# Optimization experiments

Measured on AMD Instinct MI355X. Metric: run time of the kernel, lower is better.

The kernel has to match this reference:

```python
import jax, jax.numpy as jnp
import numpy as np

KERNELS = (9, 7, 5, 3)


def setup_inputs() -> dict:
    key = jax.random.key(0)
    ks = jax.random.split(key, 10)
    Nx = Ny = 512
    D = 256
    C = 8192
    H = 1024
    T = 5
    S = len(KERNELS)
    sc = 0.05
    node_emb = jax.random.normal(ks[0], (Nx * Ny, D), jnp.float32)
    tile_ids = jax.random.randint(ks[1], (C,), 0, Nx * Ny)
    cm = jax.random.randint(ks[2], (C, T), 0, 2, dtype=jnp.int32)
    create_mask = cm.at[:, 0].set(1)  # guarantee every city is eligible
    return dict(
        node_emb=node_emb,
        conv_W0=jax.random.normal(ks[3], (S, D, D), jnp.float32) * sc,
        conv_b0=jnp.zeros((S, D), jnp.float32),
        conv_W1=jax.random.normal(ks[4], (S, D, D), jnp.float32) * sc,
        conv_b1=jnp.zeros((S, D), jnp.float32),
        mlp_W0=jax.random.normal(ks[5], (D * (1 + S), H), jnp.float32) * sc,
        mlp_b0=jnp.zeros((H,), jnp.float32),
        mlp_W1=jax.random.normal(ks[6], (H, H), jnp.float32) * sc,
        mlp_b1=jnp.zeros((H,), jnp.float32),
        mlp_W2=jax.random.normal(ks[7], (H, T), jnp.float32) * sc,
        mlp_b2=jnp.zeros((T,), jnp.float32),
        tile_ids=tile_ids,
        create_mask=create_mask,
        Nx=Nx,
        Ny=Ny,
    )


def _forward(node_emb, conv_W0, conv_b0, conv_W1, conv_b1,
             mlp_W0, mlp_b0, mlp_W1, mlp_b1, mlp_W2, mlp_b2,
             tile_ids, create_mask, Nx, Ny):
    D = node_emb.shape[1]
    rmax = max(KERNELS) // 2
    # zero-padded spatial grid, matching F.unfold with padding=k//2
    grid = node_emb.reshape(Nx, Ny, D)
    padded = jnp.pad(grid, ((rmax, rmax), (rmax, rmax), (0, 0)))
    Wp = Ny + 2 * rmax
    pf = padded.reshape(-1, D)  # (padded_tiles, D)
    x = tile_ids // Ny
    y = tile_ids % Ny
    feats = [node_emb[tile_ids]]  # (C, D) raw city embedding
    for s, k in enumerate(KERNELS):
        r = k // 2
        off = jnp.arange(-r, r + 1)
        ix = x[:, None, None] + off[None, :, None] + rmax  # (C,k,1)
        iy = y[:, None, None] + off[None, None, :] + rmax  # (C,1,k)
        flat = ix * Wp + iy  # (C,k,k)
        pooled = pf[flat].mean(axis=(1, 2))  # (C,D) mean-pooled patch
        h = jax.nn.relu(pooled @ conv_W0[s] + conv_b0[s])
        h = h @ conv_W1[s] + conv_b1[s]  # n_conv_layers=2 projection
        feats.append(h)
    combined = jnp.concatenate(feats, axis=-1)  # (C, D*(1+S))
    h = jax.nn.relu(combined @ mlp_W0 + mlp_b0)
    h = jax.nn.relu(h @ mlp_W1 + mlp_b1)
    logits = h @ mlp_W2 + mlp_b2  # (C, T)
    mask = create_mask > 0
    # stable masked softmax
    neg_inf = jnp.array(-jnp.inf, logits.dtype)
    m = jnp.max(jnp.where(mask, logits, neg_inf), axis=-1, keepdims=True)
    e = jnp.where(mask, jnp.exp(logits - m), 0.0)
    probs = e / jnp.sum(e, axis=-1, keepdims=True)
    safe = jnp.clip(probs, 1e-8, None)
    entropies = -jnp.sum(probs * jnp.log(safe), axis=-1)
    logits_masked = jnp.where(mask, logits, neg_inf)
    return probs, entropies, logits_masked, mask


def reference(node_emb, conv_W0, conv_b0, conv_W1, conv_b1,
              mlp_W0, mlp_b0, mlp_W1, mlp_b1, mlp_W2, mlp_b2,
              tile_ids, create_mask, Nx, Ny):
    return _forward(node_emb, conv_W0, conv_b0, conv_W1, conv_b1,
                    mlp_W0, mlp_b0, mlp_W1, mlp_b1, mlp_W2, mlp_b2,
                    tile_ids, create_mask, Nx, Ny)
```

## Files before the change

kernel.cpp:

```cpp
#include <hip/hip_runtime.h>
#include <hip/hip_bf16.h>
#include <math.h>
#include <float.h>

#define NX 512
#define NY 512
#define DIM 256
#define CITIES 8192
#define HID 1024
#define TT 5
#define NS 4
#define COMB (DIM * (1 + NS))

typedef unsigned short u16;
typedef __attribute__((ext_vector_type(8))) short short8;
typedef __attribute__((ext_vector_type(8))) unsigned short ushort8;
typedef __attribute__((ext_vector_type(4))) float f32x4;

__device__ __forceinline__ u16 f2bf(float f) {
    __hip_bfloat16 h = __float2bfloat16(f);
    return __builtin_bit_cast(u16, h);
}
__device__ __forceinline__ float bf2f(u16 u) {
    __hip_bfloat16 h = __builtin_bit_cast(__hip_bfloat16, u);
    return __bfloat162float(h);
}

__global__ __launch_bounds__(256)
void transpose_bf16(const float* __restrict__ in, u16* __restrict__ out,
                    int K, int N) {
    __shared__ float tile[32][33];
    const int s = blockIdx.z;
    in  += (size_t)s * K * N;
    out += (size_t)s * K * N;
    const int bn = blockIdx.x * 32, bk = blockIdx.y * 32;
    const int tx = threadIdx.x & 31, ty = threadIdx.x >> 5;
#pragma unroll
    for (int i = 0; i < 32; i += 8)
        tile[ty + i][tx] = in[(size_t)(bk + ty + i) * N + bn + tx];
    __syncthreads();
#pragma unroll
    for (int i = 0; i < 32; i += 8)
        out[(size_t)(bn + ty + i) * K + bk + tx] = f2bf(tile[tx][ty + i]);
}

__global__ void pool_kernel(const float* __restrict__ node_emb,
                            const int* __restrict__ tile_ids,
                            u16* __restrict__ P,
                            u16* __restrict__ combined) {
    int c = blockIdx.x;
    int d = threadIdx.x;
    int tile = tile_ids[c];
    int x = tile >> 9;
    int y = tile & 511;
    float s3 = 0.f, s5 = 0.f, s7 = 0.f, s9 = 0.f, center = 0.f;
#pragma unroll
    for (int dx = -4; dx <= 4; ++dx) {
        int gx = x + dx;
        bool okx = ((unsigned)gx < (unsigned)NX);
#pragma unroll
        for (int dy = -4; dy <= 4; ++dy) {
            int gy = y + dy;
            float v = 0.f;
            if (okx && ((unsigned)gy < (unsigned)NY)) {
                v = node_emb[(size_t)((gx << 9) + gy) * DIM + d];
            }
            s9 += v;
            const int ax = dx < 0 ? -dx : dx;
            const int ay = dy < 0 ? -dy : dy;
            if (ax <= 3 && ay <= 3) s7 += v;
            if (ax <= 2 && ay <= 2) s5 += v;
            if (ax <= 1 && ay <= 1) s3 += v;
            if (dx == 0 && dy == 0) center = v;
        }
    }
    combined[(size_t)c * COMB + d] = f2bf(center);
    P[((size_t)c * NS + 0) * DIM + d] = f2bf(s9 * (1.f / 81.f));
    P[((size_t)c * NS + 1) * DIM + d] = f2bf(s7 * (1.f / 49.f));
    P[((size_t)c * NS + 2) * DIM + d] = f2bf(s5 * (1.f / 25.f));
    P[((size_t)c * NS + 3) * DIM + d] = f2bf(s3 * (1.f / 9.f));
}

__global__ __launch_bounds__(256)
void gemm_bf16(const u16* __restrict__ A, int lda, long aZ,
               const u16* __restrict__ BT, int ldb, long bZ,
               const float* __restrict__ bias, long biasZ,
               u16* __restrict__ C, int ldc, long cZ,
               int K, int relu) {
    __shared__ u16 ldsA[128 * 64];
    __shared__ u16 ldsB[128 * 64];
    A    += (size_t)blockIdx.z * aZ;
    BT   += (size_t)blockIdx.z * bZ;
    bias += (size_t)blockIdx.z * biasZ;
    C    += (size_t)blockIdx.z * cZ;

    const int t    = threadIdx.x;
    const int lane = t & 63;
    const int wid  = t >> 6;
    const int wm   = wid >> 1;
    const int wn   = wid & 1;
    const int m0   = blockIdx.y * 128;
    const int n0   = blockIdx.x * 128;

    const int srow0 = wid * 32 + (lane >> 3);
    const int c7    = lane & 7;
    const int fr    = lane & 15;
    const int kq    = lane >> 4;

    f32x4 acc[4][4];
#pragma unroll
    for (int m = 0; m < 4; ++m)
#pragma unroll
        for (int n = 0; n < 4; ++n) acc[m][n] = (f32x4){0.f, 0.f, 0.f, 0.f};

    for (int k0 = 0; k0 < K; k0 += 64) {
        __syncthreads();
#pragma unroll
        for (int i = 0; i < 4; ++i) {
            const int row = srow0 + i * 8;
            const int sc  = c7 ^ (row & 7);
            const u16* ga = A + (size_t)(m0 + row) * lda + k0 + sc * 8;
            __builtin_amdgcn_global_load_lds(
                (const __attribute__((address_space(1))) void*)ga,
                (__attribute__((address_space(3))) void*)(ldsA + (wid * 32 + i * 8) * 64),
                16, 0, 0);
        }
#pragma unroll
        for (int i = 0; i < 4; ++i) {
            const int row = srow0 + i * 8;
            const int sc  = c7 ^ (row & 7);
            const u16* gb = BT + (size_t)(n0 + row) * ldb + k0 + sc * 8;
            __builtin_amdgcn_global_load_lds(
                (const __attribute__((address_space(1))) void*)gb,
                (__attribute__((address_space(3))) void*)(ldsB + (wid * 32 + i * 8) * 64),
                16, 0, 0);
        }
        __syncthreads();

#pragma unroll
        for (int kk = 0; kk < 2; ++kk) {
            short8 af[4], bfr[4];
#pragma unroll
            for (int m = 0; m < 4; ++m) {
                const int r  = wm * 64 + m * 16 + fr;
                const int ck = (kk * 4 + kq) ^ (r & 7);
                af[m] = *(const short8*)(ldsA + r * 64 + ck * 8);
            }
#pragma unroll
            for (int n = 0; n < 4; ++n) {
                const int r  = wn * 64 + n * 16 + fr;
                const int ck = (kk * 4 + kq) ^ (r & 7);
                bfr[n] = *(const short8*)(ldsB + r * 64 + ck * 8);
            }
#pragma unroll
            for (int m = 0; m < 4; ++m)
#pragma unroll
                for (int n = 0; n < 4; ++n)
                    acc[m][n] = __builtin_amdgcn_mfma_f32_16x16x32_bf16(
                        af[m], bfr[n], acc[m][n], 0, 0, 0);
        }
    }

#pragma unroll
    for (int n = 0; n < 4; ++n) {
        const int col = n0 + wn * 64 + n * 16 + fr;
        const float bv = bias[col];
#pragma unroll
        for (int m = 0; m < 4; ++m) {
            const int row = m0 + wm * 64 + m * 16 + kq * 4;
#pragma unroll
            for (int r = 0; r < 4; ++r) {
                float v = acc[m][n][r] + bv;
                if (relu) v = fmaxf(v, 0.f);
                C[(size_t)(row + r) * ldc + col] = f2bf(v);
            }
        }
    }
}

__global__ __launch_bounds__(256)
void logits_kernel(const u16* __restrict__ g2,
                   const float* __restrict__ W2,
                   const float* __restrict__ b2,
                   float* __restrict__ logits) {
    int row  = blockIdx.x * 4 + (threadIdx.x >> 6);
    int lane = threadIdx.x & 63;
    const u16* gr = g2 + (size_t)row * HID + lane * 16;
    ushort8 v0 = *(const ushort8*)(gr);
    ushort8 v1 = *(const ushort8*)(gr + 8);
    float acc[TT] = {0.f, 0.f, 0.f, 0.f, 0.f};
    const int kbase = lane * 16;
#pragma unroll
    for (int e = 0; e < 8; ++e) {
        float g = bf2f(v0[e]);
#pragma unroll
        for (int tt = 0; tt < TT; ++tt) acc[tt] += g * W2[(kbase + e) * TT + tt];
    }
#pragma unroll
    for (int e = 0; e < 8; ++e) {
        float g = bf2f(v1[e]);
#pragma unroll
        for (int tt = 0; tt < TT; ++tt) acc[tt] += g * W2[(kbase + 8 + e) * TT + tt];
    }
#pragma unroll
    for (int off = 32; off > 0; off >>= 1) {
#pragma unroll
        for (int tt = 0; tt < TT; ++tt)
            acc[tt] += __shfl_down(acc[tt], off, 64);
    }
    if (lane == 0) {
#pragma unroll
        for (int tt = 0; tt < TT; ++tt)
            logits[(size_t)row * TT + tt] = acc[tt] + b2[tt];
    }
}

__global__ void softmax_kernel(const float* __restrict__ logits,
                               const int* __restrict__ create_mask,
                               float* __restrict__ out) {
    int c = blockIdx.x * blockDim.x + threadIdx.x;
    if (c >= CITIES) return;
    float l[TT];
    int mk[TT];
#pragma unroll
    for (int tt = 0; tt < TT; ++tt) {
        l[tt] = logits[(size_t)c * TT + tt];
        mk[tt] = create_mask[(size_t)c * TT + tt];
    }
    float m = -INFINITY;
#pragma unroll
    for (int tt = 0; tt < TT; ++tt)
        if (mk[tt]) m = fmaxf(m, l[tt]);
    float e[TT];
    float s = 0.f;
#pragma unroll
    for (int tt = 0; tt < TT; ++tt) {
        e[tt] = mk[tt] ? expf(l[tt] - m) : 0.f;
        s += e[tt];
    }
    float inv = 1.f / s;
    float ent = 0.f;
    float* probs   = out;
    float* entrop  = out + (size_t)5 * CITIES;
    float* lmasked = out + (size_t)6 * CITIES;
    float* maskout = out + (size_t)11 * CITIES;
#pragma unroll
    for (int tt = 0; tt < TT; ++tt) {
        float p = e[tt] * inv;
        probs[(size_t)c * TT + tt] = p;
        ent -= p * logf(fmaxf(p, 1e-8f));
        lmasked[(size_t)c * TT + tt] = mk[tt] ? l[tt] : -1e30f;
        maskout[(size_t)c * TT + tt] = mk[tt] ? 1.f : 0.f;
    }
    entrop[c] = ent;
}

extern "C" void kernel_launch(void* const* d_in, const int* in_sizes, int n_in,
                              void* d_out, int out_size, void* d_ws, size_t ws_size,
                              hipStream_t stream) {
    const float* node_emb = (const float*)d_in[0];
    const float* conv_W0  = (const float*)d_in[1];
    const float* conv_b0  = (const float*)d_in[2];
    const float* conv_W1  = (const float*)d_in[3];
    const float* conv_b1  = (const float*)d_in[4];
    const float* mlp_W0   = (const float*)d_in[5];
    const float* mlp_b0   = (const float*)d_in[6];
    const float* mlp_W1   = (const float*)d_in[7];
    const float* mlp_b1   = (const float*)d_in[8];
    const float* mlp_W2   = (const float*)d_in[9];
    const float* mlp_b2   = (const float*)d_in[10];
    const int*   tile_ids = (const int*)d_in[11];
    const int*   cmask    = (const int*)d_in[12];
    float* out = (float*)d_out;

    char* w = (char*)d_ws;
    u16* P_bf   = (u16*)w;                    w += (size_t)CITIES * NS * DIM * 2;
    u16* comb   = (u16*)w;                    w += (size_t)CITIES * COMB * 2;
    u16* h0     = (u16*)w;                    w += (size_t)CITIES * NS * DIM * 2;
    u16* g1     = (u16*)w;                    w += (size_t)CITIES * HID * 2;
    u16* g2     = (u16*)w;                    w += (size_t)CITIES * HID * 2;
    u16* W0T    = (u16*)w;                    w += (size_t)NS * DIM * DIM * 2;
    u16* W1T    = (u16*)w;                    w += (size_t)NS * DIM * DIM * 2;
    u16* Wm0T   = (u16*)w;                    w += (size_t)HID * COMB * 2;
    u16* Wm1T   = (u16*)w;                    w += (size_t)HID * HID * 2;
    float* logits = (float*)w;                w += (size_t)CITIES * TT * 4;

    transpose_bf16<<<dim3(DIM/32, DIM/32, NS), 256, 0, stream>>>(conv_W0, W0T, DIM, DIM);
    transpose_bf16<<<dim3(DIM/32, DIM/32, NS), 256, 0, stream>>>(conv_W1, W1T, DIM, DIM);
    transpose_bf16<<<dim3(HID/32, COMB/32, 1), 256, 0, stream>>>(mlp_W0, Wm0T, COMB, HID);
    transpose_bf16<<<dim3(HID/32, HID/32, 1), 256, 0, stream>>>(mlp_W1, Wm1T, HID, HID);

    pool_kernel<<<CITIES, DIM, 0, stream>>>(node_emb, tile_ids, P_bf, comb);

    gemm_bf16<<<dim3(DIM/128, CITIES/128, NS), 256, 0, stream>>>(
        P_bf, NS * DIM, DIM,
        W0T, DIM, (long)DIM * DIM,
        conv_b0, DIM,
        h0, NS * DIM, DIM,
        DIM, 1);
    gemm_bf16<<<dim3(DIM/128, CITIES/128, NS), 256, 0, stream>>>(
        h0, NS * DIM, DIM,
        W1T, DIM, (long)DIM * DIM,
        conv_b1, DIM,
        comb + DIM, COMB, DIM,
        DIM, 0);

    gemm_bf16<<<dim3(HID/128, CITIES/128, 1), 256, 0, stream>>>(
        comb, COMB, 0,
        Wm0T, COMB, 0,
        mlp_b0, 0,
        g1, HID, 0,
        COMB, 1);
    gemm_bf16<<<dim3(HID/128, CITIES/128, 1), 256, 0, stream>>>(
        g1, HID, 0,
        Wm1T, HID, 0,
        mlp_b1, 0,
        g2, HID, 0,
        HID, 1);

    logits_kernel<<<CITIES / 4, 256, 0, stream>>>(g2, mlp_W2, mlp_b2, logits);

    softmax_kernel<<<(CITIES + 255) / 256, 256, 0, stream>>>(logits, cmask, out);
}
```

Baseline: 544.5 us.

## Merge weight transposes, vectorize pooling, swizzle GEMM blocks, fuse logits with softmax

After: 531.5 us. 2.4% less time.

```diff
diff --git a/kernel.cpp b/kernel.cpp
--- a/kernel.cpp
+++ b/kernel.cpp
@@ -15,6 +15,7 @@
 typedef unsigned short u16;
 typedef __attribute__((ext_vector_type(8))) short short8;
 typedef __attribute__((ext_vector_type(8))) unsigned short ushort8;
+typedef __attribute__((ext_vector_type(4))) unsigned short ushort4v;
 typedef __attribute__((ext_vector_type(4))) float f32x4;
 
 __device__ __forceinline__ u16 f2bf(float f) {
@@ -27,33 +28,60 @@
 }
 
 __global__ __launch_bounds__(256)
-void transpose_bf16(const float* __restrict__ in, u16* __restrict__ out,
-                    int K, int N) {
+void prep_weights(const float* __restrict__ cW0, const float* __restrict__ cW1,
+                  const float* __restrict__ mW0, const float* __restrict__ mW1,
+                  u16* __restrict__ W0T, u16* __restrict__ W1T,
+                  u16* __restrict__ Wm0T, u16* __restrict__ Wm1T) {
     __shared__ float tile[32][33];
-    const int s = blockIdx.z;
-    in  += (size_t)s * K * N;
-    out += (size_t)s * K * N;
-    const int bn = blockIdx.x * 32, bk = blockIdx.y * 32;
+    const int bid = blockIdx.x;
+    const float* src;
+    u16* dst;
+    int K, N, bn, bk;
+    if (bid < 512) {
+        const float* s0 = (bid < 256) ? cW0 : cW1;
+        u16* d0 = (bid < 256) ? W0T : W1T;
+        int b = bid & 255;
+        int batch = b >> 6;
+        int t = b & 63;
+        src = s0 + (size_t)batch * DIM * DIM;
+        dst = d0 + (size_t)batch * DIM * DIM;
+        K = DIM; N = DIM;
+        bn = (t & 7) * 32;
+        bk = (t >> 3) * 32;
+    } else if (bid < 512 + 1280) {
+        int b = bid - 512;
+        src = mW0; dst = Wm0T; K = COMB; N = HID;
+        bn = (b & 31) * 32;
+        bk = (b >> 5) * 32;
+    } else {
+        int b = bid - 1792;
+        src = mW1; dst = Wm1T; K = HID; N = HID;
+        bn = (b & 31) * 32;
+        bk = (b >> 5) * 32;
+    }
     const int tx = threadIdx.x & 31, ty = threadIdx.x >> 5;
 #pragma unroll
     for (int i = 0; i < 32; i += 8)
-        tile[ty + i][tx] = in[(size_t)(bk + ty + i) * N + bn + tx];
+        tile[ty + i][tx] = src[(size_t)(bk + ty + i) * N + bn + tx];
     __syncthreads();
 #pragma unroll
     for (int i = 0; i < 32; i += 8)
-        out[(size_t)(bn + ty + i) * K + bk + tx] = f2bf(tile[tx][ty + i]);
-}
-
-__global__ void pool_kernel(const float* __restrict__ node_emb,
-                            const int* __restrict__ tile_ids,
-                            u16* __restrict__ P,
-                            u16* __restrict__ combined) {
-    int c = blockIdx.x;
-    int d = threadIdx.x;
-    int tile = tile_ids[c];
-    int x = tile >> 9;
-    int y = tile & 511;
-    float s3 = 0.f, s5 = 0.f, s7 = 0.f, s9 = 0.f, center = 0.f;
+        dst[(size_t)(bn + ty + i) * K + bk + tx] = f2bf(tile[tx][ty + i]);
+}
+
+__global__ __launch_bounds__(256)
+void pool_kernel(const float* __restrict__ node_emb,
+                 const int* __restrict__ tile_ids,
+                 u16* __restrict__ P,
+                 u16* __restrict__ combined) {
+    const int w    = threadIdx.x >> 6;
+    const int lane = threadIdx.x & 63;
+    const int c    = blockIdx.x * 4 + w;
+    const int tile = tile_ids[c];
+    const int x = tile >> 9;
+    const int y = tile & 511;
+    f32x4 s3 = {0,0,0,0}, s5 = {0,0,0,0}, s7 = {0,0,0,0}, s9 = {0,0,0,0};
+    f32x4 ctr = {0,0,0,0};
 #pragma unroll
     for (int dx = -4; dx <= 4; ++dx) {
         int gx = x + dx;
@@ -61,9 +89,10 @@
 #pragma unroll
         for (int dy = -4; dy <= 4; ++dy) {
             int gy = y + dy;
-            float v = 0.f;
+            f32x4 v = {0,0,0,0};
             if (okx && ((unsigned)gy < (unsigned)NY)) {
-                v = node_emb[(size_t)((gx << 9) + gy) * DIM + d];
+                v = *((const f32x4*)&node_emb[(size_t)((gx << 9) + gy) * DIM]
+                      + lane);
             }
             s9 += v;
             const int ax = dx < 0 ? -dx : dx;
@@ -71,14 +100,19 @@
             if (ax <= 3 && ay <= 3) s7 += v;
             if (ax <= 2 && ay <= 2) s5 += v;
             if (ax <= 1 && ay <= 1) s3 += v;
-            if (dx == 0 && dy == 0) center = v;
-        }
-    }
-    combined[(size_t)c * COMB + d] = f2bf(center);
-    P[((size_t)c * NS + 0) * DIM + d] = f2bf(s9 * (1.f / 81.f));
-    P[((size_t)c * NS + 1) * DIM + d] = f2bf(s7 * (1.f / 49.f));
-    P[((size_t)c * NS + 2) * DIM + d] = f2bf(s5 * (1.f / 25.f));
-    P[((size_t)c * NS + 3) * DIM + d] = f2bf(s3 * (1.f / 9.f));
+            if (dx == 0 && dy == 0) ctr = v;
+        }
+    }
+    auto pack = [](f32x4 v) {
+        ushort4v r;
+        r.x = f2bf(v.x); r.y = f2bf(v.y); r.z = f2bf(v.z); r.w = f2bf(v.w);
+        return r;
+    };
+    *(ushort4v*)&combined[(size_t)c * COMB + lane * 4] = pack(ctr);
+    *(ushort4v*)&P[((size_t)c * NS + 0) * DIM + lane * 4] = pack(s9 * (1.f / 81.f));
+    *(ushort4v*)&P[((size_t)c * NS + 1) * DIM + lane * 4] = pack(s7 * (1.f / 49.f));
+    *(ushort4v*)&P[((size_t)c * NS + 2) * DIM + lane * 4] = pack(s5 * (1.f / 25.f));
+    *(ushort4v*)&P[((size_t)c * NS + 3) * DIM + lane * 4] = pack(s3 * (1.f / 9.f));
 }
 
 __global__ __launch_bounds__(256)
@@ -94,13 +128,25 @@
     bias += (size_t)blockIdx.z * biasZ;
     C    += (size_t)blockIdx.z * cZ;
 
+    int bx = blockIdx.x, by = blockIdx.y;
+    {
+        const int nwg = gridDim.x * gridDim.y;
+        if ((nwg & 7) == 0) {
+            const int bid = by * gridDim.x + bx;
+            const int cpx = nwg >> 3;
+            const int swz = (bid & 7) * cpx + (bid >> 3);
+            bx = swz % gridDim.x;
+            by = swz / gridDim.x;
+        }
+    }
+
     const int t    = threadIdx.x;
     const int lane = t & 63;
     const int wid  = t >> 6;
     const int wm   = wid >> 1;
     const int wn   = wid & 1;
-    const int m0   = blockIdx.y * 128;
-    const int n0   = blockIdx.x * 128;
+    const int m0   = by * 128;
+    const int n0   = bx * 128;
 
     const int srow0 = wid * 32 + (lane >> 3);
     const int c7    = lane & 7;
@@ -179,13 +225,15 @@
 }
 
 __global__ __launch_bounds__(256)
-void logits_kernel(const u16* __restrict__ g2,
-                   const float* __restrict__ W2,
-                   const float* __restrict__ b2,
-                   float* __restrict__ logits) {
-    int row  = blockIdx.x * 4 + (threadIdx.x >> 6);
-    int lane = threadIdx.x & 63;
-    const u16* gr = g2 + (size_t)row * HID + lane * 16;
+void head_kernel(const u16* __restrict__ g2,
+                 const float* __restrict__ W2,
+                 const float* __restrict__ b2,
+                 const int* __restrict__ create_mask,
+                 float* __restrict__ out) {
+    const int w    = threadIdx.x >> 6;
+    const int lane = threadIdx.x & 63;
+    const int c    = blockIdx.x * 4 + w;
+    const u16* gr = g2 + (size_t)c * HID + lane * 16;
     ushort8 v0 = *(const ushort8*)(gr);
     ushort8 v1 = *(const ushort8*)(gr + 8);
     float acc[TT] = {0.f, 0.f, 0.f, 0.f, 0.f};
@@ -209,50 +257,40 @@
             acc[tt] += __shfl_down(acc[tt], off, 64);
     }
     if (lane == 0) {
+        float l[TT];
+        int mk[TT];
+#pragma unroll
+        for (int tt = 0; tt < TT; ++tt) {
+            l[tt]  = acc[tt] + b2[tt];
+            mk[tt] = create_mask[(size_t)c * TT + tt];
+        }
+        float m = -INFINITY;
 #pragma unroll
         for (int tt = 0; tt < TT; ++tt)
-            logits[(size_t)row * TT + tt] = acc[tt] + b2[tt];
-    }
-}
-
-__global__ void softmax_kernel(const float* __restrict__ logits,
-                               const int* __restrict__ create_mask,
-                               float* __restrict__ out) {
-    int c = blockIdx.x * blockDim.x + threadIdx.x;
-    if (c >= CITIES) return;
-    float l[TT];
-    int mk[TT];
-#pragma unroll
-    for (int tt = 0; tt < TT; ++tt) {
-        l[tt] = logits[(size_t)c * TT + tt];
-        mk[tt] = create_mask[(size_t)c * TT + tt];
-    }
-    float m = -INFINITY;
-#pragma unroll
-    for (int tt = 0; tt < TT; ++tt)
-        if (mk[tt]) m = fmaxf(m, l[tt]);
-    float e[TT];
-    float s = 0.f;
-#pragma unroll
-    for (int tt = 0; tt < TT; ++tt) {
-        e[tt] = mk[tt] ? expf(l[tt] - m) : 0.f;
-        s += e[tt];
-    }
-    float inv = 1.f / s;
-    float ent = 0.f;
-    float* probs   = out;
-    float* entrop  = out + (size_t)5 * CITIES;
-    float* lmasked = out + (size_t)6 * CITIES;
-    float* maskout = out + (size_t)11 * CITIES;
-#pragma unroll
-    for (int tt = 0; tt < TT; ++tt) {
-        float p = e[tt] * inv;
-        probs[(size_t)c * TT + tt] = p;
-        ent -= p * logf(fmaxf(p, 1e-8f));
-        lmasked[(size_t)c * TT + tt] = mk[tt] ? l[tt] : -1e30f;
-        maskout[(size_t)c * TT + tt] = mk[tt] ? 1.f : 0.f;
-    }
-    entrop[c] = ent;
+            if (mk[tt]) m = fmaxf(m, l[tt]);
+        float e[TT];
+        float s = 0.f;
+#pragma unroll
+        for (int tt = 0; tt < TT; ++tt) {
+            e[tt] = mk[tt] ? expf(l[tt] - m) : 0.f;
+            s += e[tt];
+        }
+        float inv = 1.f / s;
+        float ent = 0.f;
+        float* probs   = out;
+        float* entrop  = out + (size_t)5 * CITIES;
+        float* lmasked = out + (size_t)6 * CITIES;
+        float* maskout = out + (size_t)11 * CITIES;
+#pragma unroll
+        for (int tt = 0; tt < TT; ++tt) {
+            float p = e[tt] * inv;
+            probs[(size_t)c * TT + tt] = p;
+            ent -= p * logf(fmaxf(p, 1e-8f));
+            lmasked[(size_t)c * TT + tt] = mk[tt] ? l[tt] : -1e30f;
+            maskout[(size_t)c * TT + tt] = mk[tt] ? 1.f : 0.f;
+        }
+        entrop[c] = ent;
+    }
 }
 
 extern "C" void kernel_launch(void* const* d_in, const int* in_sizes, int n_in,
@@ -283,14 +321,11 @@
     u16* W1T    = (u16*)w;                    w += (size_t)NS * DIM * DIM * 2;
     u16* Wm0T   = (u16*)w;                    w += (size_t)HID * COMB * 2;
     u16* Wm1T   = (u16*)w;                    w += (size_t)HID * HID * 2;
-    float* logits = (float*)w;                w += (size_t)CITIES * TT * 4;
-
-    transpose_bf16<<<dim3(DIM/32, DIM/32, NS), 256, 0, stream>>>(conv_W0, W0T, DIM, DIM);
-    transpose_bf16<<<dim3(DIM/32, DIM/32, NS), 256, 0, stream>>>(conv_W1, W1T, DIM, DIM);
-    transpose_bf16<<<dim3(HID/32, COMB/32, 1), 256, 0, stream>>>(mlp_W0, Wm0T, COMB, HID);
-    transpose_bf16<<<dim3(HID/32, HID/32, 1), 256, 0, stream>>>(mlp_W1, Wm1T, HID, HID);
-
-    pool_kernel<<<CITIES, DIM, 0, stream>>>(node_emb, tile_ids, P_bf, comb);
+
+    prep_weights<<<2816, 256, 0, stream>>>(conv_W0, conv_W1, mlp_W0, mlp_W1,
+                                           W0T, W1T, Wm0T, Wm1T);
+
+    pool_kernel<<<CITIES / 4, 256, 0, stream>>>(node_emb, tile_ids, P_bf, comb);
 
     gemm_bf16<<<dim3(DIM/128, CITIES/128, NS), 256, 0, stream>>>(
         P_bf, NS * DIM, DIM,
@@ -318,7 +353,5 @@
         g2, HID, 0,
         HID, 1);
 
-    logits_kernel<<<CITIES / 4, 256, 0, stream>>>(g2, mlp_W2, mlp_b2, logits);
-
-    softmax_kernel<<<(CITIES + 255) / 256, 256, 0, stream>>>(logits, cmask, out);
-}
+    head_kernel<<<CITIES / 4, 256, 0, stream>>>(g2, mlp_W2, mlp_b2, cmask, out);
+}
```
